# Kernel optimization log

Hardware: AMD Instinct MI355X
Metric: run time of the kernel (lower is better)

## Reference

```python
import jax, jax.numpy as jnp
import numpy as np

C = 256
C8 = C // 8


def setup_inputs() -> dict:
    key = jax.random.key(0)
    ks = jax.random.split(key, 9)
    B, H, W = 4, 64, 64
    inp = jax.random.normal(ks[0], (B, C, H, W), dtype=jnp.float32)
    original = jax.random.normal(ks[1], (B, C, H, W), dtype=jnp.float32)
    s = 1.0 / np.sqrt(C)
    wq = jax.random.normal(ks[2], (C8, C), dtype=jnp.float32) * s
    bq = jax.random.normal(ks[3], (C8,), dtype=jnp.float32) * 0.01
    wk = jax.random.normal(ks[4], (C8, C), dtype=jnp.float32) * s
    bk = jax.random.normal(ks[5], (C8,), dtype=jnp.float32) * 0.01
    wv = jax.random.normal(ks[6], (C, C), dtype=jnp.float32) * s
    bv = jax.random.normal(ks[7], (C,), dtype=jnp.float32) * 0.01
    # torch inits gamma to 0; use a nonzero value so the attention branch contributes
    gamma = jnp.asarray([0.5], dtype=jnp.float32)
    return {"input": inp, "original": original, "wq": wq, "bq": bq,
            "wk": wk, "bk": bk, "wv": wv, "bv": bv, "gamma": gamma}


def reference(input, original, wq, bq, wk, bk, wv, bv, gamma):
    B, Cc, H, W = input.shape
    HW = H * W
    x = input.reshape(B, Cc, HW)          # [B, C, HW]
    o = original.reshape(B, Cc, HW)
    # 1x1 convs == per-pixel linear projections
    q = jnp.einsum('oc,bcn->bno', wq, x) + bq          # [B, HW, C8]
    k = jnp.einsum('oc,bcn->bon', wk, x) + bk[:, None]  # [B, C8, HW]
    v = jnp.einsum('oc,bcn->bon', wv, o) + bv[:, None]  # [B, C, HW]
    attn = jax.nn.softmax(jnp.einsum('bic,bcj->bij', q, k), axis=-1)  # [B, HW, HW]
    out = jnp.einsum('bcj,bij->bci', v, attn)           # [B, C, HW]
    out = out.reshape(B, Cc, H, W)
    return gamma[0] * out + input
```

## Files before the change

kernel.cpp:

```cpp
#include <hip/hip_runtime.h>

typedef short s16x8 __attribute__((ext_vector_type(8)));
typedef float f32x4 __attribute__((ext_vector_type(4)));
typedef float f32x16 __attribute__((ext_vector_type(16)));

#define B_ 4
#define C_ 256
#define S_ 4096
#define LOG2E 1.44269504088896f
#define M2 32.0f

#if __has_builtin(__builtin_amdgcn_exp2f)
#define EXP2(x) __builtin_amdgcn_exp2f(x)
#else
#define EXP2(x) __exp2f(x)
#endif

__device__ __forceinline__ unsigned short f2b(float f) {
  union { float f; unsigned u; } v; v.f = f;
  unsigned r = v.u + 0x7fffu + ((v.u >> 16) & 1u);
  return (unsigned short)(r >> 16);
}
__device__ __forceinline__ unsigned short f2b_fast(float f) {
  union { float f; unsigned u; } v; v.f = f;
  return (unsigned short)((v.u + 0x8000u) >> 16);
}
#define PK2(x, y) ((unsigned)f2b_fast(x) | ((unsigned)f2b_fast(y) << 16))
__device__ __forceinline__ s16x8 lds_ld8(const unsigned short* p) {
  union { s16x8 v; uint2 u[2]; } r;
  r.u[0] = *(const uint2*)p;
  r.u[1] = *(const uint2*)(p + 4);
  return r.v;
}

__global__ __launch_bounds__(256)
void proj_kernel(const float* __restrict__ x, const float* __restrict__ orig,
                 const float* __restrict__ wq, const float* __restrict__ bq,
                 const float* __restrict__ wk, const float* __restrict__ bk,
                 const float* __restrict__ wv, const float* __restrict__ bv,
                 unsigned short* __restrict__ Qb, unsigned short* __restrict__ Kb,
                 unsigned short* __restrict__ Vf) {
  __shared__ unsigned short Al[64 * 68];
  __shared__ unsigned short Sl[64 * 68];
  const int ct = blockIdx.x >> 6;
  const int jt = blockIdx.x & 63;
  const int n0 = jt * 64;
  const int b  = blockIdx.y;
  const int t  = threadIdx.x;
  const int L = t & 63, w = t >> 6;
  const int mt = w >> 1, nt = w & 1;
  const int g = L >> 5, l32 = L & 31;
  const float* srcb = ((ct == 0) ? x : orig) + (size_t)b * C_ * S_;
  f32x16 acc = (f32x16)0.0f;

  for (int kc = 0; kc < 4; ++kc) {
    const int k0 = kc * 64;
    __syncthreads();
    #pragma unroll
    for (int rep = 0; rep < 4; ++rep) {
      const int idx = rep * 256 + t;
      const int row = idx >> 4, c4 = (idx & 15) * 4;
      const float* wsrc; int wrow;
      if (ct == 0) {
        if (row < 32) { wsrc = wq; wrow = row; } else { wsrc = wk; wrow = row - 32; }
      } else { wsrc = wv; wrow = (ct - 1) * 64 + row; }
      f32x4 v = *(const f32x4*)(wsrc + (size_t)wrow * 256 + k0 + c4);
      union { unsigned short us[4]; uint2 u2; } pk;
      #pragma unroll
      for (int i = 0; i < 4; ++i) pk.us[i] = f2b(v[i]);
      *(uint2*)&Al[row * 68 + c4] = pk.u2;
    }
    {
      const int c4 = (t >> 4) * 4;
      const int n4 = (t & 15) * 4;
      f32x4 v0 = *(const f32x4*)(srcb + (size_t)(k0 + c4 + 0) * S_ + n0 + n4);
      f32x4 v1 = *(const f32x4*)(srcb + (size_t)(k0 + c4 + 1) * S_ + n0 + n4);
      f32x4 v2 = *(const f32x4*)(srcb + (size_t)(k0 + c4 + 2) * S_ + n0 + n4);
      f32x4 v3 = *(const f32x4*)(srcb + (size_t)(k0 + c4 + 3) * S_ + n0 + n4);
      #pragma unroll
      for (int k = 0; k < 4; ++k) {
        union { unsigned short us[4]; uint2 u2; } pk;
        pk.us[0] = f2b(v0[k]); pk.us[1] = f2b(v1[k]);
        pk.us[2] = f2b(v2[k]); pk.us[3] = f2b(v3[k]);
        *(uint2*)&Sl[(n4 + k) * 68 + c4] = pk.u2;
      }
    }
    __syncthreads();
    #pragma unroll
    for (int ks = 0; ks < 4; ++ks) {
      s16x8 af = lds_ld8(&Al[(mt * 32 + l32) * 68 + ks * 16 + g * 8]);
      s16x8 bf = lds_ld8(&Sl[(nt * 32 + l32) * 68 + ks * 16 + g * 8]);
      acc = __builtin_amdgcn_mfma_f32_32x32x16_bf16(af, bf, acc, 0, 0, 0);
    }
  }
  __syncthreads();
  unsigned short* Rl = Al;
  const int n = nt * 32 + l32;
  if (ct == 0) {
    #pragma unroll
    for (int reg = 0; reg < 16; ++reg) {
      const int rr = (reg & 3) + 8 * (reg >> 2) + 4 * g;
      const float val = (mt == 0) ? (acc[reg] + bq[rr]) * LOG2E : acc[reg] + bk[rr];
      Rl[n * 68 + mt * 32 + rr] = f2b(val);
    }
    __syncthreads();
    const int nn = t >> 2, ch0 = (t & 3) * 16;
    s16x8 a = lds_ld8(Rl + nn * 68 + ch0);
    s16x8 c = lds_ld8(Rl + nn * 68 + ch0 + 8);
    unsigned short* dst = (ch0 < 32)
        ? Qb + ((size_t)b * S_ + n0 + nn) * 32 + ch0
        : Kb + ((size_t)b * S_ + n0 + nn) * 32 + (ch0 - 32);
    *(s16x8*)dst = a;
    *(s16x8*)(dst + 8) = c;
  } else {
    const int cg = ct - 1;
    #pragma unroll
    for (int reg = 0; reg < 16; ++reg) {
      const int rr = (reg & 3) + 8 * (reg >> 2) + 4 * g;
      const int ch = mt * 32 + rr;
      Rl[ch * 68 + n] = f2b(acc[reg] + bv[cg * 64 + ch]);
    }
    __syncthreads();
    #pragma unroll
    for (int k = 0; k < 2; ++k) {
      const int G = t * 2 + k;
      const int t2 = G >> 8;
      const int gh = (G >> 7) & 1;
      const int s  = (G >> 6) & 1;
      const int Lf = G & 63;
      const int hh = Lf >> 5;
      const int ch_l = gh * 32 + (Lf & 31);
      const int jloc = t2 * 32 + s * 16 + hh * 4;
      uint2 q0 = *(const uint2*)&Rl[ch_l * 68 + jloc];
      uint2 q1 = *(const uint2*)&Rl[ch_l * 68 + jloc + 8];
      unsigned short* dst = Vf + (((size_t)(b * 128 + jt * 2 + t2) * 8)
                                  + cg * 2 + gh) * 1024 + s * 512 + (size_t)Lf * 8;
      *(uint2*)dst = q0;
      *(uint2*)(dst + 4) = q1;
    }
  }
}


#define MFMA32(A, B, C) __builtin_amdgcn_mfma_f32_32x32x16_bf16(A, B, C, 0, 0, 0)

#define LOADV(JT)                                                               \
  {                                                                             \
    const unsigned short* vb = Vf + (((size_t)(b * 128 + (JT)) * 8)             \
                                     + chh * 4) * 1024 + (size_t)L * 8;         \
    v00 = *(const s16x8*)(vb + 0 * 1024);                                       \
    v01 = *(const s16x8*)(vb + 0 * 1024 + 512);                                 \
    v10 = *(const s16x8*)(vb + 1 * 1024);                                       \
    v11 = *(const s16x8*)(vb + 1 * 1024 + 512);                                 \
    v20 = *(const s16x8*)(vb + 2 * 1024);                                       \
    v21 = *(const s16x8*)(vb + 2 * 1024 + 512);                                 \
    v30 = *(const s16x8*)(vb + 3 * 1024);                                       \
    v31 = *(const s16x8*)(vb + 3 * 1024 + 512);                                 \
  }

#define DO_IG(QF0, QF1, A0, A1, A2, A3, LPV)                                    \
  {                                                                             \
    f32x16 p = MFMA32(kc0, QF0, cinit);                                         \
    p = MFMA32(kc1, QF1, p);                                                    \
    const float e0 = EXP2(p[0]),  e1 = EXP2(p[1]),  e2 = EXP2(p[2]),  e3 = EXP2(p[3]);   \
    const float e4 = EXP2(p[4]),  e5 = EXP2(p[5]),  e6 = EXP2(p[6]),  e7 = EXP2(p[7]);   \
    const float e8 = EXP2(p[8]),  e9 = EXP2(p[9]),  e10 = EXP2(p[10]), e11 = EXP2(p[11]); \
    const float e12 = EXP2(p[12]), e13 = EXP2(p[13]), e14 = EXP2(p[14]), e15 = EXP2(p[15]); \
    LPV += (((e0 + e1) + (e2 + e3)) + ((e4 + e5) + (e6 + e7)))                  \
         + (((e8 + e9) + (e10 + e11)) + ((e12 + e13) + (e14 + e15)));           \
    union { unsigned u[4]; s16x8 v; } pa, pb;                                   \
    pa.u[0] = PK2(e0, e1);   pa.u[1] = PK2(e2, e3);                             \
    pa.u[2] = PK2(e4, e5);   pa.u[3] = PK2(e6, e7);                             \
    pb.u[0] = PK2(e8, e9);   pb.u[1] = PK2(e10, e11);                           \
    pb.u[2] = PK2(e12, e13); pb.u[3] = PK2(e14, e15);                           \
    A0 = MFMA32(pa.v, v00, A0);  A0 = MFMA32(pb.v, v01, A0);                    \
    A1 = MFMA32(pa.v, v10, A1);  A1 = MFMA32(pb.v, v11, A1);                    \
    A2 = MFMA32(pa.v, v20, A2);  A2 = MFMA32(pb.v, v21, A2);                    \
    A3 = MFMA32(pa.v, v30, A3);  A3 = MFMA32(pb.v, v31, A3);                    \
  }

#define DUMP_ADD(ACC, IG, CG)                                                   \
  _Pragma("unroll")                                                             \
  for (int r = 0; r < 16; ++r) {                                                \
    const int rr = (r & 3) + 8 * (r >> 2) + 4 * h;                              \
    scr[(IG) * 32 + rr][chh * 128 + (CG) * 32 + l31] += ACC[r];                 \
  }

__global__ __launch_bounds__(512, 2)
void flash_kernel(const unsigned short* __restrict__ Qb,
                  const unsigned short* __restrict__ Kb,
                  const unsigned short* __restrict__ Vf,
                  const float* __restrict__ inp,
                  const float* __restrict__ gamma,
                  float* __restrict__ out) {
  __shared__ float scr[64][260];
  __shared__ float lpart[4][64];
  __shared__ float invl[64];
  const int l  = blockIdx.x;
  const int b  = (l & 7) >> 1;
  const int i0 = ((l >> 3) * 2 + (l & 1)) * 64;
  const int t  = threadIdx.x;
  const int L = t & 63, w = t >> 6;
  const int l31 = L & 31, h = L >> 5;
  const int jq = w >> 1, chh = w & 1;
  const float gam = gamma[0];
  const unsigned short* Kbase = Kb + (size_t)b * S_ * 32;

  {
    float* sf = &scr[0][0];
    for (int z = t; z < 64 * 260; z += 512) sf[z] = 0.0f;
  }

  const s16x8 qf00 = *(const s16x8*)(Qb + ((size_t)b * S_ + i0 + l31) * 32 + h * 8);
  const s16x8 qf01 = *(const s16x8*)(Qb + ((size_t)b * S_ + i0 + l31) * 32 + 16 + h * 8);
  const s16x8 qf10 = *(const s16x8*)(Qb + ((size_t)b * S_ + i0 + 32 + l31) * 32 + h * 8);
  const s16x8 qf11 = *(const s16x8*)(Qb + ((size_t)b * S_ + i0 + 32 + l31) * 32 + 16 + h * 8);

  f32x16 a00 = (f32x16)0.0f, a01 = (f32x16)0.0f, a02 = (f32x16)0.0f, a03 = (f32x16)0.0f;
  f32x16 a10 = (f32x16)0.0f, a11 = (f32x16)0.0f, a12 = (f32x16)0.0f, a13 = (f32x16)0.0f;
  float lp0 = 0.f, lp1 = 0.f;
  const f32x16 cinit = (f32x16)(-M2);

  s16x8 kc0, kc1, kn0, kn1;
  s16x8 v00, v01, v10, v11, v20, v21, v30, v31;
  {
    const int jt0 = jq * 32;
    kc0 = *(const s16x8*)(Kbase + (size_t)(jt0 * 32 + l31) * 32 + h * 8);
    kc1 = *(const s16x8*)(Kbase + (size_t)(jt0 * 32 + l31) * 32 + 16 + h * 8);
  }

  for (int st = 0; st < 32; ++st) {
    const int jt = jq * 32 + st;
    LOADV(jt);
    DO_IG(qf00, qf01, a00, a01, a02, a03, lp0);
    {
      const int jn = (jt + 1 < 128) ? jt + 1 : 127;
      kn0 = *(const s16x8*)(Kbase + (size_t)(jn * 32 + l31) * 32 + h * 8);
      kn1 = *(const s16x8*)(Kbase + (size_t)(jn * 32 + l31) * 32 + 16 + h * 8);
    }
    DO_IG(qf10, qf11, a10, a11, a12, a13, lp1);
    kc0 = kn0; kc1 = kn1;
  }

  lp0 += __shfl_xor(lp0, 32, 64);
  lp1 += __shfl_xor(lp1, 32, 64);
  if (chh == 0 && L < 32) {
    lpart[jq][L] = lp0;
    lpart[jq][32 + L] = lp1;
  }
  #pragma unroll 1
  for (int ph = 0; ph < 4; ++ph) {
    __syncthreads();
    if (jq == ph) {
      DUMP_ADD(a00, 0, 0); DUMP_ADD(a01, 0, 1); DUMP_ADD(a02, 0, 2); DUMP_ADD(a03, 0, 3);
      DUMP_ADD(a10, 1, 0); DUMP_ADD(a11, 1, 1); DUMP_ADD(a12, 1, 2); DUMP_ADD(a13, 1, 3);
    }
  }
  __syncthreads();
  if (t < 64) invl[t] = gam / (lpart[0][t] + lpart[1][t] + lpart[2][t] + lpart[3][t]);
  __syncthreads();
  {
    const int ch = t >> 1;
    const int ih = (t & 1) * 32;
    #pragma unroll
    for (int q = 0; q < 8; ++q) {
      const int il = ih + q * 4;
      const size_t gi = ((size_t)b * C_ + ch) * S_ + i0 + il;
      const f32x4 iv = *(const f32x4*)(inp + gi);
      f32x4 o;
      #pragma unroll
      for (int k = 0; k < 4; ++k)
        o[k] = scr[il + k][ch] * invl[il + k] + iv[k];
      *(f32x4*)(out + gi) = o;
    }
  }
}

extern "C" void kernel_launch(void* const* d_in, const int* in_sizes, int n_in,
                              void* d_out, int out_size, void* d_ws, size_t ws_size,
                              hipStream_t stream) {
  const float* inp   = (const float*)d_in[0];
  const float* orig  = (const float*)d_in[1];
  const float* wq    = (const float*)d_in[2];
  const float* bq    = (const float*)d_in[3];
  const float* wk    = (const float*)d_in[4];
  const float* bk    = (const float*)d_in[5];
  const float* wv    = (const float*)d_in[6];
  const float* bv    = (const float*)d_in[7];
  const float* gamma = (const float*)d_in[8];
  float* out = (float*)d_out;

  unsigned short* Qb = (unsigned short*)d_ws;
  unsigned short* Kb = Qb + (size_t)B_ * S_ * 32;
  unsigned short* Vf = Kb + (size_t)B_ * S_ * 32;

  proj_kernel<<<dim3(320, 4), 256, 0, stream>>>(inp, orig, wq, bq, wk, bk, wv, bv, Qb, Kb, Vf);
  flash_kernel<<<256, 512, 0, stream>>>(Qb, Kb, Vf, inp, gamma, out);
}
```

Measured before the change: 158.0 us.

## Halve flash block query tile to 32 rows with 4 waves and twice the blocks

Each flash-attention block now handles 32 query rows instead of 64. It uses 256 threads (2 key halves × 2 channel halves), and the grid is doubled to 512 blocks. Each wave keeps one query group instead of two, which removes half the accumulators and cuts register and LDS pressure per block. The cost is that the V and K fragments loaded each step are reused across only one query group, so global/L2 traffic per unit of MFMA work roughly doubles. The epilogue indexing is reworked to match the smaller tile.

```diff
diff --git a/kernel.cpp b/kernel.cpp
--- a/kernel.cpp
+++ b/kernel.cpp
@@ -158,119 +158,105 @@
     v31 = *(const s16x8*)(vb + 3 * 1024 + 512);                                 \
   }
 
-#define DO_IG(QF0, QF1, A0, A1, A2, A3, LPV)                                    \
-  {                                                                             \
-    f32x16 p = MFMA32(kc0, QF0, cinit);                                         \
-    p = MFMA32(kc1, QF1, p);                                                    \
-    const float e0 = EXP2(p[0]),  e1 = EXP2(p[1]),  e2 = EXP2(p[2]),  e3 = EXP2(p[3]);   \
-    const float e4 = EXP2(p[4]),  e5 = EXP2(p[5]),  e6 = EXP2(p[6]),  e7 = EXP2(p[7]);   \
-    const float e8 = EXP2(p[8]),  e9 = EXP2(p[9]),  e10 = EXP2(p[10]), e11 = EXP2(p[11]); \
-    const float e12 = EXP2(p[12]), e13 = EXP2(p[13]), e14 = EXP2(p[14]), e15 = EXP2(p[15]); \
-    LPV += (((e0 + e1) + (e2 + e3)) + ((e4 + e5) + (e6 + e7)))                  \
-         + (((e8 + e9) + (e10 + e11)) + ((e12 + e13) + (e14 + e15)));           \
-    union { unsigned u[4]; s16x8 v; } pa, pb;                                   \
-    pa.u[0] = PK2(e0, e1);   pa.u[1] = PK2(e2, e3);                             \
-    pa.u[2] = PK2(e4, e5);   pa.u[3] = PK2(e6, e7);                             \
-    pb.u[0] = PK2(e8, e9);   pb.u[1] = PK2(e10, e11);                           \
-    pb.u[2] = PK2(e12, e13); pb.u[3] = PK2(e14, e15);                           \
-    A0 = MFMA32(pa.v, v00, A0);  A0 = MFMA32(pb.v, v01, A0);                    \
-    A1 = MFMA32(pa.v, v10, A1);  A1 = MFMA32(pb.v, v11, A1);                    \
-    A2 = MFMA32(pa.v, v20, A2);  A2 = MFMA32(pb.v, v21, A2);                    \
-    A3 = MFMA32(pa.v, v30, A3);  A3 = MFMA32(pb.v, v31, A3);                    \
-  }
-
-#define DUMP_ADD(ACC, IG, CG)                                                   \
-  _Pragma("unroll")                                                             \
-  for (int r = 0; r < 16; ++r) {                                                \
-    const int rr = (r & 3) + 8 * (r >> 2) + 4 * h;                              \
-    scr[(IG) * 32 + rr][chh * 128 + (CG) * 32 + l31] += ACC[r];                 \
-  }
-
-__global__ __launch_bounds__(512, 2)
+__global__ __launch_bounds__(256, 3)
 void flash_kernel(const unsigned short* __restrict__ Qb,
                   const unsigned short* __restrict__ Kb,
                   const unsigned short* __restrict__ Vf,
                   const float* __restrict__ inp,
                   const float* __restrict__ gamma,
                   float* __restrict__ out) {
-  __shared__ float scr[64][260];
-  __shared__ float lpart[4][64];
-  __shared__ float invl[64];
+  __shared__ float scr[32][260];
+  __shared__ float lpart[2][32];
+  __shared__ float invl[32];
   const int l  = blockIdx.x;
   const int b  = (l & 7) >> 1;
-  const int i0 = ((l >> 3) * 2 + (l & 1)) * 64;
+  const int i0 = ((l >> 3) * 2 + (l & 1)) * 32;
   const int t  = threadIdx.x;
   const int L = t & 63, w = t >> 6;
   const int l31 = L & 31, h = L >> 5;
-  const int jq = w >> 1, chh = w & 1;
+  const int jq = w & 1, chh = w >> 1;
   const float gam = gamma[0];
   const unsigned short* Kbase = Kb + (size_t)b * S_ * 32;
 
   {
     float* sf = &scr[0][0];
-    for (int z = t; z < 64 * 260; z += 512) sf[z] = 0.0f;
-  }
-
-  const s16x8 qf00 = *(const s16x8*)(Qb + ((size_t)b * S_ + i0 + l31) * 32 + h * 8);
-  const s16x8 qf01 = *(const s16x8*)(Qb + ((size_t)b * S_ + i0 + l31) * 32 + 16 + h * 8);
-  const s16x8 qf10 = *(const s16x8*)(Qb + ((size_t)b * S_ + i0 + 32 + l31) * 32 + h * 8);
-  const s16x8 qf11 = *(const s16x8*)(Qb + ((size_t)b * S_ + i0 + 32 + l31) * 32 + 16 + h * 8);
-
-  f32x16 a00 = (f32x16)0.0f, a01 = (f32x16)0.0f, a02 = (f32x16)0.0f, a03 = (f32x16)0.0f;
-  f32x16 a10 = (f32x16)0.0f, a11 = (f32x16)0.0f, a12 = (f32x16)0.0f, a13 = (f32x16)0.0f;
-  float lp0 = 0.f, lp1 = 0.f;
+    for (int z = t; z < 32 * 260; z += 256) sf[z] = 0.0f;
+  }
+
+  const s16x8 qf0 = *(const s16x8*)(Qb + ((size_t)b * S_ + i0 + l31) * 32 + h * 8);
+  const s16x8 qf1 = *(const s16x8*)(Qb + ((size_t)b * S_ + i0 + l31) * 32 + 16 + h * 8);
+
+  f32x16 a0 = (f32x16)0.0f, a1 = (f32x16)0.0f, a2 = (f32x16)0.0f, a3 = (f32x16)0.0f;
+  float lpv = 0.f;
   const f32x16 cinit = (f32x16)(-M2);
 
   s16x8 kc0, kc1, kn0, kn1;
   s16x8 v00, v01, v10, v11, v20, v21, v30, v31;
   {
-    const int jt0 = jq * 32;
+    const int jt0 = jq * 64;
     kc0 = *(const s16x8*)(Kbase + (size_t)(jt0 * 32 + l31) * 32 + h * 8);
     kc1 = *(const s16x8*)(Kbase + (size_t)(jt0 * 32 + l31) * 32 + 16 + h * 8);
   }
 
-  for (int st = 0; st < 32; ++st) {
-    const int jt = jq * 32 + st;
+  for (int st = 0; st < 64; ++st) {
+    const int jt = jq * 64 + st;
     LOADV(jt);
-    DO_IG(qf00, qf01, a00, a01, a02, a03, lp0);
     {
-      const int jn = (jt + 1 < 128) ? jt + 1 : 127;
+      const int jn = (st < 63) ? jt + 1 : jt;
       kn0 = *(const s16x8*)(Kbase + (size_t)(jn * 32 + l31) * 32 + h * 8);
       kn1 = *(const s16x8*)(Kbase + (size_t)(jn * 32 + l31) * 32 + 16 + h * 8);
     }
-    DO_IG(qf10, qf11, a10, a11, a12, a13, lp1);
+    f32x16 p = MFMA32(kc0, qf0, cinit);
+    p = MFMA32(kc1, qf1, p);
+    const float e0 = EXP2(p[0]),  e1 = EXP2(p[1]),  e2 = EXP2(p[2]),  e3 = EXP2(p[3]);
+    const float e4 = EXP2(p[4]),  e5 = EXP2(p[5]),  e6 = EXP2(p[6]),  e7 = EXP2(p[7]);
+    const float e8 = EXP2(p[8]),  e9 = EXP2(p[9]),  e10 = EXP2(p[10]), e11 = EXP2(p[11]);
+    const float e12 = EXP2(p[12]), e13 = EXP2(p[13]), e14 = EXP2(p[14]), e15 = EXP2(p[15]);
+    lpv += (((e0 + e1) + (e2 + e3)) + ((e4 + e5) + (e6 + e7)))
+         + (((e8 + e9) + (e10 + e11)) + ((e12 + e13) + (e14 + e15)));
+    union { unsigned u[4]; s16x8 v; } pa, pb;
+    pa.u[0] = PK2(e0, e1);   pa.u[1] = PK2(e2, e3);
+    pa.u[2] = PK2(e4, e5);   pa.u[3] = PK2(e6, e7);
+    pb.u[0] = PK2(e8, e9);   pb.u[1] = PK2(e10, e11);
+    pb.u[2] = PK2(e12, e13); pb.u[3] = PK2(e14, e15);
+    a0 = MFMA32(pa.v, v00, a0);  a0 = MFMA32(pb.v, v01, a0);
+    a1 = MFMA32(pa.v, v10, a1);  a1 = MFMA32(pb.v, v11, a1);
+    a2 = MFMA32(pa.v, v20, a2);  a2 = MFMA32(pb.v, v21, a2);
+    a3 = MFMA32(pa.v, v30, a3);  a3 = MFMA32(pb.v, v31, a3);
     kc0 = kn0; kc1 = kn1;
   }
 
-  lp0 += __shfl_xor(lp0, 32, 64);
-  lp1 += __shfl_xor(lp1, 32, 64);
-  if (chh == 0 && L < 32) {
-    lpart[jq][L] = lp0;
-    lpart[jq][32 + L] = lp1;
-  }
+  lpv += __shfl_xor(lpv, 32, 64);
+  if (chh == 0 && L < 32) lpart[jq][L] = lpv;
   #pragma unroll 1
-  for (int ph = 0; ph < 4; ++ph) {
+  for (int ph = 0; ph < 2; ++ph) {
     __syncthreads();
     if (jq == ph) {
-      DUMP_ADD(a00, 0, 0); DUMP_ADD(a01, 0, 1); DUMP_ADD(a02, 0, 2); DUMP_ADD(a03, 0, 3);
-      DUMP_ADD(a10, 1, 0); DUMP_ADD(a11, 1, 1); DUMP_ADD(a12, 1, 2); DUMP_ADD(a13, 1, 3);
+      #pragma unroll
+      for (int r = 0; r < 16; ++r) {
+        const int rr = (r & 3) + 8 * (r >> 2) + 4 * h;
+        scr[rr][chh * 128 + 0 * 32 + l31] += a0[r];
+        scr[rr][chh * 128 + 1 * 32 + l31] += a1[r];
+        scr[rr][chh * 128 + 2 * 32 + l31] += a2[r];
+        scr[rr][chh * 128 + 3 * 32 + l31] += a3[r];
+      }
     }
   }
   __syncthreads();
-  if (t < 64) invl[t] = gam / (lpart[0][t] + lpart[1][t] + lpart[2][t] + lpart[3][t]);
+  if (t < 32) invl[t] = gam / (lpart[0][t] + lpart[1][t]);
   __syncthreads();
   {
-    const int ch = t >> 1;
-    const int ih = (t & 1) * 32;
-    #pragma unroll
-    for (int q = 0; q < 8; ++q) {
-      const int il = ih + q * 4;
-      const size_t gi = ((size_t)b * C_ + ch) * S_ + i0 + il;
+    const int chq = t >> 3;
+    const int i4  = (t & 7) * 4;
+    #pragma unroll
+    for (int cc = 0; cc < 8; ++cc) {
+      const int ch = cc * 32 + chq;
+      const size_t gi = ((size_t)b * C_ + ch) * S_ + i0 + i4;
       const f32x4 iv = *(const f32x4*)(inp + gi);
       f32x4 o;
       #pragma unroll
       for (int k = 0; k < 4; ++k)
-        o[k] = scr[il + k][ch] * invl[il + k] + iv[k];
+        o[k] = scr[i4 + k][ch] * invl[i4 + k] + iv[k];
       *(f32x4*)(out + gi) = o;
     }
   }
@@ -295,5 +281,5 @@
   unsigned short* Vf = Kb + (size_t)B_ * S_ * 32;
 
   proj_kernel<<<dim3(320, 4), 256, 0, stream>>>(inp, orig, wq, bq, wk, bk, wv, bv, Qb, Kb, Vf);
-  flash_kernel<<<256, 512, 0, stream>>>(Qb, Kb, Vf, inp, gamma, out);
-}
+  flash_kernel<<<512, 256, 0, stream>>>(Qb, Kb, Vf, inp, gamma, out);
+}
```

New measurement: 161.8 us. +2.4%, slower.

## Pre-convert projection weights to bf16 once and stage full-K activation tile

Applied to the files above, without the earlier changes.

Adds a small prep kernel that converts the Q/K/V weights to bf16 once, folds the log2e scale into Wq and bq, and packs the Q/K biases. The projection kernel then reads weight fragments straight from global memory instead of staging them through LDS. It also loads the whole 256-channel activation tile into LDS with a single barrier, replacing the four K-chunk iterations that each needed two barriers. The cost is one extra kernel launch, a larger LDS footprint per block, and global weight reads from every wave; folding the scale before bf16 rounding also changes numerics slightly.

```diff
diff --git a/kernel.cpp b/kernel.cpp
--- a/kernel.cpp
+++ b/kernel.cpp
@@ -34,14 +34,33 @@
 }
 
 __global__ __launch_bounds__(256)
+void prep_kernel(const float* __restrict__ wq, const float* __restrict__ bq,
+                 const float* __restrict__ wk, const float* __restrict__ bk,
+                 const float* __restrict__ wv,
+                 unsigned short* __restrict__ Wb, float* __restrict__ bqk) {
+  const int t = threadIdx.x;
+  const int r = blockIdx.x * 4 + (t >> 6);
+  const int c4 = (t & 63) * 4;
+  const float* src; float scale = 1.0f;
+  if (r < 32)      { src = wq + (size_t)r * 256;        scale = LOG2E; }
+  else if (r < 64) { src = wk + (size_t)(r - 32) * 256; }
+  else             { src = wv + (size_t)(r - 64) * 256; }
+  f32x4 v = *(const f32x4*)(src + c4);
+  union { unsigned short us[4]; uint2 u2; } pk;
+  #pragma unroll
+  for (int i = 0; i < 4; ++i) pk.us[i] = f2b(v[i] * scale);
+  *(uint2*)&Wb[(size_t)r * 256 + c4] = pk.u2;
+  if (blockIdx.x == 0 && t < 64) bqk[t] = (t < 32) ? bq[t] * LOG2E : bk[t - 32];
+}
+
+__global__ __launch_bounds__(256)
 void proj_kernel(const float* __restrict__ x, const float* __restrict__ orig,
-                 const float* __restrict__ wq, const float* __restrict__ bq,
-                 const float* __restrict__ wk, const float* __restrict__ bk,
-                 const float* __restrict__ wv, const float* __restrict__ bv,
+                 const unsigned short* __restrict__ Wb,
+                 const float* __restrict__ bqk, const float* __restrict__ bv,
                  unsigned short* __restrict__ Qb, unsigned short* __restrict__ Kb,
                  unsigned short* __restrict__ Vf) {
-  __shared__ unsigned short Al[64 * 68];
-  __shared__ unsigned short Sl[64 * 68];
+  __shared__ unsigned short Sl[64 * 260];
+  __shared__ unsigned short Rl[64 * 68];
   const int ct = blockIdx.x >> 6;
   const int jt = blockIdx.x & 63;
   const int n0 = jt * 64;
@@ -51,28 +70,13 @@
   const int mt = w >> 1, nt = w & 1;
   const int g = L >> 5, l32 = L & 31;
   const float* srcb = ((ct == 0) ? x : orig) + (size_t)b * C_ * S_;
-  f32x16 acc = (f32x16)0.0f;
-
-  for (int kc = 0; kc < 4; ++kc) {
-    const int k0 = kc * 64;
-    __syncthreads();
-    #pragma unroll
-    for (int rep = 0; rep < 4; ++rep) {
-      const int idx = rep * 256 + t;
-      const int row = idx >> 4, c4 = (idx & 15) * 4;
-      const float* wsrc; int wrow;
-      if (ct == 0) {
-        if (row < 32) { wsrc = wq; wrow = row; } else { wsrc = wk; wrow = row - 32; }
-      } else { wsrc = wv; wrow = (ct - 1) * 64 + row; }
-      f32x4 v = *(const f32x4*)(wsrc + (size_t)wrow * 256 + k0 + c4);
-      union { unsigned short us[4]; uint2 u2; } pk;
-      #pragma unroll
-      for (int i = 0; i < 4; ++i) pk.us[i] = f2b(v[i]);
-      *(uint2*)&Al[row * 68 + c4] = pk.u2;
-    }
-    {
-      const int c4 = (t >> 4) * 4;
-      const int n4 = (t & 15) * 4;
+
+  {
+    const int c4 = (t >> 4) * 4;
+    const int n4 = (t & 15) * 4;
+    #pragma unroll
+    for (int kc = 0; kc < 4; ++kc) {
+      const int k0 = kc * 64;
       f32x4 v0 = *(const f32x4*)(srcb + (size_t)(k0 + c4 + 0) * S_ + n0 + n4);
       f32x4 v1 = *(const f32x4*)(srcb + (size_t)(k0 + c4 + 1) * S_ + n0 + n4);
       f32x4 v2 = *(const f32x4*)(srcb + (size_t)(k0 + c4 + 2) * S_ + n0 + n4);
@@ -82,26 +86,31 @@
         union { unsigned short us[4]; uint2 u2; } pk;
         pk.us[0] = f2b(v0[k]); pk.us[1] = f2b(v1[k]);
         pk.us[2] = f2b(v2[k]); pk.us[3] = f2b(v3[k]);
-        *(uint2*)&Sl[(n4 + k) * 68 + c4] = pk.u2;
+        *(uint2*)&Sl[(n4 + k) * 260 + k0 + c4] = pk.u2;
       }
     }
-    __syncthreads();
+  }
+  __syncthreads();
+
+  const int wrow0 = (ct == 0) ? (mt * 32 + l32) : (64 + (ct - 1) * 64 + mt * 32 + l32);
+  const unsigned short* Wr = Wb + (size_t)wrow0 * 256;
+  f32x16 acc = (f32x16)0.0f;
+  #pragma unroll
+  for (int kc = 0; kc < 4; ++kc) {
     #pragma unroll
     for (int ks = 0; ks < 4; ++ks) {
-      s16x8 af = lds_ld8(&Al[(mt * 32 + l32) * 68 + ks * 16 + g * 8]);
-      s16x8 bf = lds_ld8(&Sl[(nt * 32 + l32) * 68 + ks * 16 + g * 8]);
+      const s16x8 af = *(const s16x8*)(Wr + kc * 64 + ks * 16 + g * 8);
+      const s16x8 bf = lds_ld8(&Sl[(nt * 32 + l32) * 260 + kc * 64 + ks * 16 + g * 8]);
       acc = __builtin_amdgcn_mfma_f32_32x32x16_bf16(af, bf, acc, 0, 0, 0);
     }
   }
-  __syncthreads();
-  unsigned short* Rl = Al;
+
   const int n = nt * 32 + l32;
   if (ct == 0) {
     #pragma unroll
     for (int reg = 0; reg < 16; ++reg) {
       const int rr = (reg & 3) + 8 * (reg >> 2) + 4 * g;
-      const float val = (mt == 0) ? (acc[reg] + bq[rr]) * LOG2E : acc[reg] + bk[rr];
-      Rl[n * 68 + mt * 32 + rr] = f2b(val);
+      Rl[n * 68 + mt * 32 + rr] = f2b(acc[reg] + bqk[mt * 32 + rr]);
     }
     __syncthreads();
     const int nn = t >> 2, ch0 = (t & 3) * 16;
@@ -293,7 +302,10 @@
   unsigned short* Qb = (unsigned short*)d_ws;
   unsigned short* Kb = Qb + (size_t)B_ * S_ * 32;
   unsigned short* Vf = Kb + (size_t)B_ * S_ * 32;
-
-  proj_kernel<<<dim3(320, 4), 256, 0, stream>>>(inp, orig, wq, bq, wk, bk, wv, bv, Qb, Kb, Vf);
+  unsigned short* Wb = Vf + (size_t)B_ * 128 * 8 * 1024;
+  float* bqk = (float*)(Wb + 320 * 256);
+
+  prep_kernel<<<80, 256, 0, stream>>>(wq, bq, wk, bk, wv, Wb, bqk);
+  proj_kernel<<<dim3(320, 4), 256, 0, stream>>>(inp, orig, Wb, bqk, bv, Qb, Kb, Vf);
   flash_kernel<<<256, 512, 0, stream>>>(Qb, Kb, Vf, inp, gamma, out);
 }
```

Result: slower. 164.4 us (+4.1%).
